# Kernel optimization log

Hardware: AMD Instinct MI355X
Metric: run time of the kernel (lower is better)

Reference implementation:

```python
import jax, jax.numpy as jnp
import numpy as np

N = 100000      # nodes
E = 1600000     # edges
C_IN = 128
H = 64          # hidden_channels
FC = [128, 64, 32, 16]
G = 64          # graphs in batch
EPS = 1e-5


def _glorot(key, fan_in, fan_out):
    s = 1.0 / np.sqrt(fan_in)
    return jax.random.uniform(key, (fan_in, fan_out), jnp.float32, -s, s)


def setup_inputs() -> dict:
    key = jax.random.key(0)
    ks = jax.random.split(key, 24)
    inp = {
        "x": jax.random.normal(ks[0], (N, C_IN), jnp.float32),
        "edge_index": jax.random.randint(ks[1], (2, E), 0, N, jnp.int32),
        "batch": jnp.sort(jax.random.randint(ks[2], (N,), 0, G, jnp.int32)),
        # GCN layers
        "W1": _glorot(ks[3], C_IN, H), "b1": jnp.zeros((H,), jnp.float32),
        "W2": _glorot(ks[4], H, H),    "b2": jnp.zeros((H,), jnp.float32),
        # BatchNorm affine params
        "gamma1": jnp.ones((H,), jnp.float32), "beta1": jnp.zeros((H,), jnp.float32),
        "gamma2": jnp.ones((H,), jnp.float32), "beta2": jnp.zeros((H,), jnp.float32),
        # MLP stack 64->128->64->32->16->1
        "fW1": _glorot(ks[5], H, FC[0]),     "fb1": jnp.zeros((FC[0],), jnp.float32),
        "fW2": _glorot(ks[6], FC[0], FC[1]), "fb2": jnp.zeros((FC[1],), jnp.float32),
        "fW3": _glorot(ks[7], FC[1], FC[2]), "fb3": jnp.zeros((FC[2],), jnp.float32),
        "fW4": _glorot(ks[8], FC[2], FC[3]), "fb4": jnp.zeros((FC[3],), jnp.float32),
        "oW": _glorot(ks[9], FC[3], 1),      "ob": jnp.zeros((1,), jnp.float32),
    }
    return inp


def gcn_conv(x, W, b, src, dst):
    # x' = D^{-1/2} (A + I) D^{-1/2} X W + b   (PyG GCNConv, add_self_loops=True)
    h = x @ W                                             # [N, H]
    loops = jnp.arange(N, dtype=src.dtype)
    s = jnp.concatenate([src, loops])
    d = jnp.concatenate([dst, loops])
    deg = jax.ops.segment_sum(jnp.ones_like(d, jnp.float32), d, num_segments=N)
    dinv = jax.lax.rsqrt(deg)                             # deg >= 1 (self-loops)
    norm = dinv[s] * dinv[d]                              # [E+N]
    msg = h[s] * norm[:, None]                            # gather + scale
    return jax.ops.segment_sum(msg, d, num_segments=N) + b


def batch_norm(x, gamma, beta):
    mu = jnp.mean(x, axis=0)
    var = jnp.mean((x - mu) ** 2, axis=0)                 # biased, as torch BN
    return (x - mu) * jax.lax.rsqrt(var + EPS) * gamma + beta


def reference(x, edge_index, batch, W1, b1, W2, b2, gamma1, beta1, gamma2, beta2,
              fW1, fb1, fW2, fb2, fW3, fb3, fW4, fb4, oW, ob):
    src, dst = edge_index[0], edge_index[1]
    h = jax.nn.relu(gcn_conv(x, W1, b1, src, dst))
    h = batch_norm(h, gamma1, beta1)                      # dropout = identity (eval)
    h = jax.nn.relu(gcn_conv(h, W2, b2, src, dst))
    h = batch_norm(h, gamma2, beta2)
    # global mean pool over graphs
    sums = jax.ops.segment_sum(h, batch, num_segments=G)
    cnts = jax.ops.segment_sum(jnp.ones((N,), jnp.float32), batch, num_segments=G)
    g = sums / jnp.maximum(cnts, 1.0)[:, None]            # [G, H]
    g = jax.nn.relu(g @ fW1 + fb1)
    g = jax.nn.relu(g @ fW2 + fb2)
    g = jax.nn.relu(g @ fW3 + fb3)
    g = jax.nn.relu(g @ fW4 + fb4)
    return g @ oW + ob                                    # [G, 1]
```

## Files before the change

### kernel.cpp

```cpp
#include <hip/hip_runtime.h>
#include <hip/hip_bf16.h>
#include <hip/hip_fp16.h>

#define NNODES 100000
#define NEDGES 1600000
#define NGRAPH 64
#define NCOPY  32
#define NSLOT  8

#define CAP     48
#define NGEMM1  1563

#define PSH     9
#define PSZ2    512
#define NP2     196
#define PCAP    9216
#define EPB     4096
#define NBP1    391

__global__ __launch_bounds__(1024) void k_bucket(const int* __restrict__ ei,
                                                 unsigned* __restrict__ pstage,
                                                 unsigned* __restrict__ pcur) {
    const int tid = threadIdx.x;
    __shared__ unsigned lcnt[NP2];
    __shared__ unsigned lbase[NP2];
    if (tid < NP2) lcnt[tid] = 0u;
    __syncthreads();

    int e = blockIdx.x * EPB + tid * 4;
    bool valid = (e < NEDGES);
    unsigned v0=0,v1=0,v2=0,v3=0, p0=0,p1=0,p2=0,p3=0, o0=0,o1=0,o2=0,o3=0;
    if (valid) {
        int4 sv = *reinterpret_cast<const int4*>(&ei[e]);
        int4 dv = *reinterpret_cast<const int4*>(&ei[NEDGES + e]);
        unsigned d;
        d = (unsigned)dv.x; p0 = d >> PSH; v0 = ((d & (PSZ2-1u)) << 17) | (unsigned)sv.x; o0 = atomicAdd(&lcnt[p0], 1u);
        d = (unsigned)dv.y; p1 = d >> PSH; v1 = ((d & (PSZ2-1u)) << 17) | (unsigned)sv.y; o1 = atomicAdd(&lcnt[p1], 1u);
        d = (unsigned)dv.z; p2 = d >> PSH; v2 = ((d & (PSZ2-1u)) << 17) | (unsigned)sv.z; o2 = atomicAdd(&lcnt[p2], 1u);
        d = (unsigned)dv.w; p3 = d >> PSH; v3 = ((d & (PSZ2-1u)) << 17) | (unsigned)sv.w; o3 = atomicAdd(&lcnt[p3], 1u);
    }
    __syncthreads();
    if (tid < NP2) {
        unsigned c = lcnt[tid];
        lbase[tid] = c ? atomicAdd(&pcur[tid], c) : 0u;
    }
    __syncthreads();
    if (valid) {
        unsigned i0 = lbase[p0] + o0; if (i0 < PCAP) pstage[(size_t)p0 * PCAP + i0] = v0;
        unsigned i1 = lbase[p1] + o1; if (i1 < PCAP) pstage[(size_t)p1 * PCAP + i1] = v1;
        unsigned i2 = lbase[p2] + o2; if (i2 < PCAP) pstage[(size_t)p2 * PCAP + i2] = v2;
        unsigned i3 = lbase[p3] + o3; if (i3 < PCAP) pstage[(size_t)p3 * PCAP + i3] = v3;
    }
}

__global__ __launch_bounds__(1024) void k_build(const unsigned* __restrict__ pstage,
                                                const unsigned* __restrict__ pcur,
                                                unsigned* __restrict__ cnt,
                                                float* __restrict__ dinv,
                                                unsigned* __restrict__ colidx) {
    const int p   = blockIdx.x;
    const int tid = threadIdx.x;
    __shared__ unsigned cl[PSZ2];
    if (tid < PSZ2) cl[tid] = 0u;
    __syncthreads();
    unsigned nedge = min(pcur[p], (unsigned)PCAP);
    const unsigned* q = &pstage[(size_t)p * PCAP];
    for (unsigned i = tid; i < nedge; i += 1024) {
        unsigned v    = q[i];
        unsigned r    = v >> 17;
        unsigned src  = v & 0x1FFFFu;
        unsigned slot = atomicAdd(&cl[r], 1u);
        unsigned node = ((unsigned)p << PSH) + r;
        if (slot < CAP) colidx[node * CAP + slot] = src;
    }
    __syncthreads();
    if (tid < PSZ2) {
        unsigned node = ((unsigned)p << PSH) + (unsigned)tid;
        if (node < NNODES) {
            unsigned c = cl[tid];
            cnt[node]  = c;
            dinv[node] = rsqrtf((float)(c + 1u));
        }
    }
}

__global__ __launch_bounds__(256) void k_gemm1(const float* __restrict__ A,
                                               const float* __restrict__ W,
                                               const float* __restrict__ rowscale,
                                               __half* __restrict__ hd) {
    __shared__ float wlds[64 * 64];
    __shared__ float alds[64 * 68];
    const int tid = threadIdx.x;
    const int tc = (tid & 15) * 4;
    const int tr = (tid >> 4) * 4;
    const int row0 = blockIdx.x * 64;
    float acc[4][4];
    #pragma unroll
    for (int i = 0; i < 4; ++i)
        #pragma unroll
        for (int j = 0; j < 4; ++j) acc[i][j] = 0.f;

    for (int kc = 0; kc < 2; ++kc) {
        for (int idx2 = tid; idx2 < 64 * 16; idx2 += 256) {
            int r = idx2 >> 4, kk = (idx2 & 15) * 4;
            *reinterpret_cast<float4*>(&wlds[r * 64 + kk]) =
                *reinterpret_cast<const float4*>(&W[(kc * 64 + r) * 64 + kk]);
        }
        for (int idx2 = tid; idx2 < 64 * 16; idx2 += 256) {
            int r = idx2 >> 4, kk = (idx2 & 15) * 4;
            int row = row0 + r;
            float4 v = make_float4(0.f, 0.f, 0.f, 0.f);
            if (row < NNODES) v = *reinterpret_cast<const float4*>(&A[row * 128 + kc * 64 + kk]);
            *reinterpret_cast<float4*>(&alds[r * 68 + kk]) = v;
        }
        __syncthreads();
        #pragma unroll 8
        for (int k = 0; k < 64; ++k) {
            float4 wv = *reinterpret_cast<const float4*>(&wlds[k * 64 + tc]);
            float av[4];
            #pragma unroll
            for (int i = 0; i < 4; ++i) av[i] = alds[(tr + i) * 68 + k];
            #pragma unroll
            for (int i = 0; i < 4; ++i) {
                acc[i][0] = fmaf(av[i], wv.x, acc[i][0]);
                acc[i][1] = fmaf(av[i], wv.y, acc[i][1]);
                acc[i][2] = fmaf(av[i], wv.z, acc[i][2]);
                acc[i][3] = fmaf(av[i], wv.w, acc[i][3]);
            }
        }
        __syncthreads();
    }
    #pragma unroll
    for (int i = 0; i < 4; ++i) {
        int row = row0 + tr + i;
        if (row < NNODES) {
            float f = rowscale[row];
            __half2* p = reinterpret_cast<__half2*>(&hd[(size_t)row * 64 + tc]);
            p[0] = __floats2half2_rn(acc[i][0] * f, acc[i][1] * f);
            p[1] = __floats2half2_rn(acc[i][2] * f, acc[i][3] * f);
        }
    }
}

__device__ __forceinline__ void acc_row(const __half* __restrict__ hd, unsigned s, int c0, float4& acc) {
    uint2 u = *reinterpret_cast<const uint2*>(&hd[(size_t)s * 64 + c0]);
    __half2 x01 = *reinterpret_cast<__half2*>(&u.x);
    __half2 x23 = *reinterpret_cast<__half2*>(&u.y);
    float2 f01 = __half22float2(x01);
    float2 f23 = __half22float2(x23);
    acc.x += f01.x; acc.y += f01.y; acc.z += f23.x; acc.w += f23.y;
}

#define WAVE_REDUCE_8(s0,s1,s2,s3,q0,q1,q2,q3)                      \
    {                                                                \
        _Pragma("unroll")                                            \
        for (int m = 16; m < 64; m <<= 1) {                          \
            s0 += __shfl_xor(s0, m); s1 += __shfl_xor(s1, m);        \
            s2 += __shfl_xor(s2, m); s3 += __shfl_xor(s3, m);        \
            q0 += __shfl_xor(q0, m); q1 += __shfl_xor(q1, m);        \
            q2 += __shfl_xor(q2, m); q3 += __shfl_xor(q3, m);        \
        }                                                            \
    }

__global__ __launch_bounds__(256) void k_gather_fused(const unsigned* __restrict__ cnt,
                                                      const unsigned* __restrict__ colidx,
                                                      const __half* __restrict__ hd,
                                                      const float* __restrict__ dinv,
                                                      const float* __restrict__ bias,
                                                      float* __restrict__ act,
                                                      float* bn_sum, float* bn_sq, int n) {
    const int tid = threadIdx.x;
    const int grp = tid >> 4;
    const int c0  = (tid & 15) * 4;
    float4 bv = *reinterpret_cast<const float4*>(&bias[c0]);
    float s0=0.f,s1=0.f,s2=0.f,s3=0.f, q0=0.f,q1=0.f,q2=0.f,q3=0.f;

    #pragma unroll
    for (int it = 0; it < 2; ++it) {
        int node = blockIdx.x * 32 + grp * 2 + it;
        if (node < n) {
            unsigned deg = cnt[node];
            unsigned lo = (unsigned)node * CAP;
            unsigned hi = lo + deg;
            float4 acc = make_float4(0.f, 0.f, 0.f, 0.f);
            acc_row(hd, (unsigned)node, c0, acc);
            unsigned j = lo;
            for (; j + 4 <= hi; j += 4) {
                uint4 a = *reinterpret_cast<const uint4*>(&colidx[j]);
                acc_row(hd, a.x, c0, acc);
                acc_row(hd, a.y, c0, acc);
                acc_row(hd, a.z, c0, acc);
                acc_row(hd, a.w, c0, acc);
            }
            for (; j < hi; ++j) acc_row(hd, colidx[j], c0, acc);
            float w = dinv[node];
            float4 r;
            r.x = fmaxf(fmaf(acc.x, w, bv.x), 0.f);
            r.y = fmaxf(fmaf(acc.y, w, bv.y), 0.f);
            r.z = fmaxf(fmaf(acc.z, w, bv.z), 0.f);
            r.w = fmaxf(fmaf(acc.w, w, bv.w), 0.f);
            *reinterpret_cast<float4*>(&act[(size_t)node * 64 + c0]) = r;
            s0 += r.x; s1 += r.y; s2 += r.z; s3 += r.w;
            q0 = fmaf(r.x, r.x, q0); q1 = fmaf(r.y, r.y, q1);
            q2 = fmaf(r.z, r.z, q2); q3 = fmaf(r.w, r.w, q3);
        }
    }

    WAVE_REDUCE_8(s0,s1,s2,s3,q0,q1,q2,q3);
    __shared__ float ls[4 * 64];
    __shared__ float lq[4 * 64];
    int lane = tid & 63, wid = tid >> 6;
    if (lane < 16) {
        *reinterpret_cast<float4*>(&ls[wid * 64 + lane * 4]) = make_float4(s0, s1, s2, s3);
        *reinterpret_cast<float4*>(&lq[wid * 64 + lane * 4]) = make_float4(q0, q1, q2, q3);
    }
    __syncthreads();
    if (tid < 64) {
        int cpy = (blockIdx.x & (NCOPY - 1)) * 64;
        float S = ls[tid] + ls[64 + tid] + ls[128 + tid] + ls[192 + tid];
        float Q = lq[tid] + lq[64 + tid] + lq[128 + tid] + lq[192 + tid];
        atomicAdd(&bn_sum[cpy + tid], S);
        atomicAdd(&bn_sq[cpy + tid],  Q);
    }
}

__global__ __launch_bounds__(256) void k_gather_pool(const unsigned* __restrict__ cnt,
                                                     const unsigned* __restrict__ colidx,
                                                     const __half* __restrict__ hd,
                                                     const float* __restrict__ dinv,
                                                     const float* __restrict__ bias,
                                                     const int* __restrict__ batch,
                                                     float* __restrict__ gsum,
                                                     float* bn_sum, float* bn_sq, int n) {
    const int tid = threadIdx.x;
    const int grp = tid >> 4;
    const int c0  = (tid & 15) * 4;
    float4 bv = *reinterpret_cast<const float4*>(&bias[c0]);
    float s0=0.f,s1=0.f,s2=0.f,s3=0.f, q0=0.f,q1=0.f,q2=0.f,q3=0.f;

    __shared__ float lds_pool[NSLOT * 64];
    for (int i = tid; i < NSLOT * 64; i += 256) lds_pool[i] = 0.f;
    int node0 = blockIdx.x * 32;
    int g0 = batch[node0 < n ? node0 : (n - 1)];
    __syncthreads();

    #pragma unroll
    for (int it = 0; it < 2; ++it) {
        int node = node0 + grp * 2 + it;
        if (node < n) {
            unsigned deg = cnt[node];
            unsigned lo = (unsigned)node * CAP;
            unsigned hi = lo + deg;
            float4 acc = make_float4(0.f, 0.f, 0.f, 0.f);
            acc_row(hd, (unsigned)node, c0, acc);
            unsigned j = lo;
            for (; j + 4 <= hi; j += 4) {
                uint4 a = *reinterpret_cast<const uint4*>(&colidx[j]);
                acc_row(hd, a.x, c0, acc);
                acc_row(hd, a.y, c0, acc);
                acc_row(hd, a.z, c0, acc);
                acc_row(hd, a.w, c0, acc);
            }
            for (; j < hi; ++j) acc_row(hd, colidx[j], c0, acc);
            float w = dinv[node];
            float4 r;
            r.x = fmaxf(fmaf(acc.x, w, bv.x), 0.f);
            r.y = fmaxf(fmaf(acc.y, w, bv.y), 0.f);
            r.z = fmaxf(fmaf(acc.z, w, bv.z), 0.f);
            r.w = fmaxf(fmaf(acc.w, w, bv.w), 0.f);
            s0 += r.x; s1 += r.y; s2 += r.z; s3 += r.w;
            q0 = fmaf(r.x, r.x, q0); q1 = fmaf(r.y, r.y, q1);
            q2 = fmaf(r.z, r.z, q2); q3 = fmaf(r.w, r.w, q3);
            int slot = batch[node] - g0;
            if (slot < NSLOT) {
                atomicAdd(&lds_pool[slot * 64 + c0 + 0], r.x);
                atomicAdd(&lds_pool[slot * 64 + c0 + 1], r.y);
                atomicAdd(&lds_pool[slot * 64 + c0 + 2], r.z);
                atomicAdd(&lds_pool[slot * 64 + c0 + 3], r.w);
            } else {
                int g = g0 + slot;
                atomicAdd(&gsum[g * 64 + c0 + 0], r.x);
                atomicAdd(&gsum[g * 64 + c0 + 1], r.y);
                atomicAdd(&gsum[g * 64 + c0 + 2], r.z);
                atomicAdd(&gsum[g * 64 + c0 + 3], r.w);
            }
        }
    }

    WAVE_REDUCE_8(s0,s1,s2,s3,q0,q1,q2,q3);
    __shared__ float ls[4 * 64];
    __shared__ float lq[4 * 64];
    int lane = tid & 63, wid = tid >> 6;
    if (lane < 16) {
        *reinterpret_cast<float4*>(&ls[wid * 64 + lane * 4]) = make_float4(s0, s1, s2, s3);
        *reinterpret_cast<float4*>(&lq[wid * 64 + lane * 4]) = make_float4(q0, q1, q2, q3);
    }
    __syncthreads();
    if (tid < 64) {
        int cpy = (blockIdx.x & (NCOPY - 1)) * 64;
        float S = ls[tid] + ls[64 + tid] + ls[128 + tid] + ls[192 + tid];
        float Q = lq[tid] + lq[64 + tid] + lq[128 + tid] + lq[192 + tid];
        atomicAdd(&bn_sum[cpy + tid], S);
        atomicAdd(&bn_sq[cpy + tid],  Q);
        #pragma unroll
        for (int sl = 0; sl < NSLOT; ++sl) {
            int g = g0 + sl;
            if (g < NGRAPH) {
                float v = lds_pool[sl * 64 + tid];
                if (v != 0.f) atomicAdd(&gsum[g * 64 + tid], v);
            }
        }
    }
}

__global__ void k_bn_fold_w2(const float* __restrict__ bn_sum, const float* __restrict__ bn_sq,
                             const float* __restrict__ gamma, const float* __restrict__ beta,
                             const float* __restrict__ W2, float* __restrict__ W2eff,
                             float* __restrict__ c2, int n) {
    __shared__ float sc[64], sh[64];
    int t = threadIdx.x;
    float S = 0.f, Q = 0.f;
    #pragma unroll
    for (int cpy = 0; cpy < NCOPY; ++cpy) { S += bn_sum[cpy * 64 + t]; Q += bn_sq[cpy * 64 + t]; }
    float inv_n = 1.0f / (float)n;
    float mu  = S * inv_n;
    float var = Q * inv_n - mu * mu;
    float s = gamma[t] * rsqrtf(var + 1e-5f);
    sc[t] = s; sh[t] = beta[t] - mu * s;
    __syncthreads();
    float acc = 0.f;
    for (int k = 0; k < 64; ++k) {
        float w = W2[k * 64 + t];
        W2eff[k * 64 + t] = sc[k] * w;
        acc = fmaf(sh[k], w, acc);
    }
    c2[t] = acc;
}

__global__ __launch_bounds__(256) void k_gemm64_h(const float* __restrict__ A,
                                                  const float* __restrict__ W,
                                                  const float* __restrict__ addvec,
                                                  const float* __restrict__ rowscale,
                                                  __half* __restrict__ hd, int n) {
    __shared__ float wlds[64 * 64];
    __shared__ float alds[64 * 68];
    const int tid = threadIdx.x;
    const int tc  = (tid & 15) * 4;
    const int tr  = (tid >> 4) * 4;
    const int row0 = blockIdx.x * 64;

    float acc[4][4];
    float4 cv = *reinterpret_cast<const float4*>(&addvec[tc]);
    #pragma unroll
    for (int i = 0; i < 4; ++i) { acc[i][0]=cv.x; acc[i][1]=cv.y; acc[i][2]=cv.z; acc[i][3]=cv.w; }

    {
        for (int idx = tid; idx < 64 * 16; idx += 256) {
            int r = idx >> 4, kk = (idx & 15) * 4;
            *reinterpret_cast<float4*>(&wlds[r * 64 + kk]) =
                *reinterpret_cast<const float4*>(&W[r * 64 + kk]);
        }
        for (int idx = tid; idx < 64 * 16; idx += 256) {
            int r = idx >> 4, kk = (idx & 15) * 4;
            int row = row0 + r;
            float4 v = make_float4(0.f, 0.f, 0.f, 0.f);
            if (row < n) v = *reinterpret_cast<const float4*>(&A[row * 64 + kk]);
            *reinterpret_cast<float4*>(&alds[r * 68 + kk]) = v;
        }
        __syncthreads();
        #pragma unroll 8
        for (int k = 0; k < 64; ++k) {
            float4 wv = *reinterpret_cast<const float4*>(&wlds[k * 64 + tc]);
            float av[4];
            #pragma unroll
            for (int i = 0; i < 4; ++i) av[i] = alds[(tr + i) * 68 + k];
            #pragma unroll
            for (int i = 0; i < 4; ++i) {
                acc[i][0] = fmaf(av[i], wv.x, acc[i][0]);
                acc[i][1] = fmaf(av[i], wv.y, acc[i][1]);
                acc[i][2] = fmaf(av[i], wv.z, acc[i][2]);
                acc[i][3] = fmaf(av[i], wv.w, acc[i][3]);
            }
        }
    }
    #pragma unroll
    for (int i = 0; i < 4; ++i) {
        int row = row0 + tr + i;
        if (row < n) {
            float f = rowscale[row];
            __half2* p = reinterpret_cast<__half2*>(&hd[(size_t)row * 64 + tc]);
            p[0] = __floats2half2_rn(acc[i][0] * f, acc[i][1] * f);
            p[1] = __floats2half2_rn(acc[i][2] * f, acc[i][3] * f);
        }
    }
}

__device__ __forceinline__ int lower_bound_i(const int* a, int n, int v) {
    int lo = 0, hi = n;
    while (lo < hi) { int m = (lo + hi) >> 1; if (a[m] < v) lo = m + 1; else hi = m; }
    return lo;
}
__global__ __launch_bounds__(128) void k_mlp(const float* __restrict__ gsum,
                                             const int* __restrict__ batch, int n,
                                             const float* __restrict__ bn_sum, const float* __restrict__ bn_sq,
                                             const float* __restrict__ gamma, const float* __restrict__ beta,
                                             const float* __restrict__ fW1, const float* __restrict__ fb1,
                                             const float* __restrict__ fW2, const float* __restrict__ fb2,
                                             const float* __restrict__ fW3, const float* __restrict__ fb3,
                                             const float* __restrict__ fW4, const float* __restrict__ fb4,
                                             const float* __restrict__ oW,  const float* __restrict__ ob,
                                             float* __restrict__ out) {
    int g = blockIdx.x;
    int t = threadIdx.x;
    __shared__ float a[128], bbuf[128];
    if (t < 64) {
        float S = 0.f, Q = 0.f;
        #pragma unroll
        for (int cpy = 0; cpy < NCOPY; ++cpy) { S += bn_sum[cpy * 64 + t]; Q += bn_sq[cpy * 64 + t]; }
        float inv_n = 1.0f / (float)n;
        float mu  = S * inv_n;
        float var = Q * inv_n - mu * mu;
        float s   = gamma[t] * rsqrtf(var + 1e-5f);
        float sh  = beta[t] - mu * s;
        int lo = lower_bound_i(batch, n, g);
        int hi = lower_bound_i(batch, n, g + 1);
        int cnt = hi - lo;
        a[t] = (cnt > 0) ? (gsum[g * 64 + t] / (float)cnt) * s + sh : 0.f;
    }
    __syncthreads();
    {
        float acc = fb1[t];
        for (int k = 0; k < 64; ++k) acc = fmaf(a[k], fW1[k * 128 + t], acc);
        bbuf[t] = fmaxf(acc, 0.f);
    }
    __syncthreads();
    if (t < 64) {
        float acc = fb2[t];
        for (int k = 0; k < 128; ++k) acc = fmaf(bbuf[k], fW2[k * 64 + t], acc);
        a[t] = fmaxf(acc, 0.f);
    }
    __syncthreads();
    if (t < 32) {
        float acc = fb3[t];
        for (int k = 0; k < 64; ++k) acc = fmaf(a[k], fW3[k * 32 + t], acc);
        bbuf[t] = fmaxf(acc, 0.f);
    }
    __syncthreads();
    if (t < 16) {
        float acc = fb4[t];
        for (int k = 0; k < 32; ++k) acc = fmaf(bbuf[k], fW4[k * 16 + t], acc);
        a[t] = fmaxf(acc, 0.f);
    }
    __syncthreads();
    if (t == 0) {
        float acc = ob[0];
        for (int k = 0; k < 16; ++k) acc = fmaf(a[k], oW[k], acc);
        out[g] = acc;
    }
}

extern "C" void kernel_launch(void* const* d_in, const int* in_sizes, int n_in,
                              void* d_out, int out_size, void* d_ws, size_t ws_size,
                              hipStream_t stream) {
    const float* x      = (const float*)d_in[0];
    const int*   ei     = (const int*)  d_in[1];
    const int*   batch  = (const int*)  d_in[2];
    const float* W1     = (const float*)d_in[3];
    const float* b1     = (const float*)d_in[4];
    const float* W2     = (const float*)d_in[5];
    const float* b2     = (const float*)d_in[6];
    const float* gamma1 = (const float*)d_in[7];
    const float* beta1  = (const float*)d_in[8];
    const float* gamma2 = (const float*)d_in[9];
    const float* beta2  = (const float*)d_in[10];
    const float* fW1    = (const float*)d_in[11];
    const float* fb1    = (const float*)d_in[12];
    const float* fW2    = (const float*)d_in[13];
    const float* fb2    = (const float*)d_in[14];
    const float* fW3    = (const float*)d_in[15];
    const float* fb3    = (const float*)d_in[16];
    const float* fW4    = (const float*)d_in[17];
    const float* fb4    = (const float*)d_in[18];
    const float* oW     = (const float*)d_in[19];
    const float* ob     = (const float*)d_in[20];
    float* out = (float*)d_out;

    const int N = NNODES, G = NGRAPH;

    char* base = (char*)d_ws;
    __half*   hd     = (__half*)base;
    float*    act    = (float*)(base + (size_t)N * 64 * 2);
    unsigned* cnt    = (unsigned*)((char*)act + (size_t)N * 64 * 4);
    float*    dinv   = (float*)(cnt + N);
    unsigned* colidx = (unsigned*)(dinv + N);
    float*    bn1s   = (float*)(colidx + (size_t)N * CAP);
    float*    bn1q   = bn1s + NCOPY * 64;
    float*    bn2s   = bn1q + NCOPY * 64;
    float*    bn2q   = bn2s + NCOPY * 64;
    float*    gsum   = bn2q + NCOPY * 64;
    float*    W2eff  = gsum + (size_t)G * 64;
    float*    c2     = W2eff + 4096;
    unsigned* pcur   = (unsigned*)(c2 + 64);
    unsigned* pstage = (unsigned*)act;

    hipMemsetAsync(pcur, 0, (size_t)NP2 * 4, stream);
    hipMemsetAsync(bn1s, 0, (size_t)(4 * NCOPY * 64 + G * 64) * sizeof(float), stream);

    k_bucket<<<NBP1, 1024, 0, stream>>>(ei, pstage, pcur);
    k_build<<<NP2, 1024, 0, stream>>>(pstage, pcur, cnt, dinv, colidx);

    k_gemm1<<<NGEMM1, 256, 0, stream>>>(x, W1, dinv, hd);

    k_gather_fused<<<(N + 31) / 32, 256, 0, stream>>>(cnt, colidx, hd, dinv, b1, act, bn1s, bn1q, N);
    k_bn_fold_w2<<<1, 64, 0, stream>>>(bn1s, bn1q, gamma1, beta1, W2, W2eff, c2, N);

    k_gemm64_h<<<(N + 63) / 64, 256, 0, stream>>>(act, W2eff, c2, dinv, hd, N);
    k_gather_pool<<<(N + 31) / 32, 256, 0, stream>>>(cnt, colidx, hd, dinv, b2, batch, gsum, bn2s, bn2q, N);

    k_mlp<<<G, 128, 0, stream>>>(gsum, batch, N, bn2s, bn2q, gamma2, beta2,
                                 fW1, fb1, fW2, fb2, fW3, fb3, fW4, fb4, oW, ob, out);
}
```

Baseline: 309.2 us.

## Fuse edge bucketing with GEMM1, fold BN into GEMM2, store activations in fp16

Edge bucketing and the first GEMM now run in one launch, with odd blocks doing the bucketing and even blocks doing the GEMM. Because GEMM1 no longer waits for the degree array, its source-side dinv scaling moves into the gather, which does one extra dinv load per edge. The BatchNorm fold kernel is merged into the second GEMM, and each block recomputes the scaled weights. The intermediate activation is stored in fp16 instead of fp32 to halve its traffic, and the memsets are merged. This cuts launches and serialization but adds per-edge work in the gather and some extra rounding.

```diff
diff --git a/kernel.cpp b/kernel.cpp
--- a/kernel.cpp
+++ b/kernel.cpp
@@ -15,85 +15,55 @@
 #define PSZ2    512
 #define NP2     196
 #define PCAP    9216
-#define EPB     4096
-#define NBP1    391
-
-__global__ __launch_bounds__(1024) void k_bucket(const int* __restrict__ ei,
-                                                 unsigned* __restrict__ pstage,
-                                                 unsigned* __restrict__ pcur) {
+
+__global__ __launch_bounds__(256) void k_bucket_gemm1(const float* __restrict__ A,
+                                                      const float* __restrict__ W,
+                                                      const int* __restrict__ ei,
+                                                      unsigned* __restrict__ pstage,
+                                                      unsigned* __restrict__ pcur,
+                                                      __half* __restrict__ hd) {
+    __shared__ __align__(16) float smem[64 * 64 + 64 * 68];
+    const int b   = blockIdx.x;
     const int tid = threadIdx.x;
-    __shared__ unsigned lcnt[NP2];
-    __shared__ unsigned lbase[NP2];
-    if (tid < NP2) lcnt[tid] = 0u;
-    __syncthreads();
-
-    int e = blockIdx.x * EPB + tid * 4;
-    bool valid = (e < NEDGES);
-    unsigned v0=0,v1=0,v2=0,v3=0, p0=0,p1=0,p2=0,p3=0, o0=0,o1=0,o2=0,o3=0;
-    if (valid) {
-        int4 sv = *reinterpret_cast<const int4*>(&ei[e]);
-        int4 dv = *reinterpret_cast<const int4*>(&ei[NEDGES + e]);
-        unsigned d;
-        d = (unsigned)dv.x; p0 = d >> PSH; v0 = ((d & (PSZ2-1u)) << 17) | (unsigned)sv.x; o0 = atomicAdd(&lcnt[p0], 1u);
-        d = (unsigned)dv.y; p1 = d >> PSH; v1 = ((d & (PSZ2-1u)) << 17) | (unsigned)sv.y; o1 = atomicAdd(&lcnt[p1], 1u);
-        d = (unsigned)dv.z; p2 = d >> PSH; v2 = ((d & (PSZ2-1u)) << 17) | (unsigned)sv.z; o2 = atomicAdd(&lcnt[p2], 1u);
-        d = (unsigned)dv.w; p3 = d >> PSH; v3 = ((d & (PSZ2-1u)) << 17) | (unsigned)sv.w; o3 = atomicAdd(&lcnt[p3], 1u);
-    }
-    __syncthreads();
-    if (tid < NP2) {
-        unsigned c = lcnt[tid];
-        lbase[tid] = c ? atomicAdd(&pcur[tid], c) : 0u;
-    }
-    __syncthreads();
-    if (valid) {
-        unsigned i0 = lbase[p0] + o0; if (i0 < PCAP) pstage[(size_t)p0 * PCAP + i0] = v0;
-        unsigned i1 = lbase[p1] + o1; if (i1 < PCAP) pstage[(size_t)p1 * PCAP + i1] = v1;
-        unsigned i2 = lbase[p2] + o2; if (i2 < PCAP) pstage[(size_t)p2 * PCAP + i2] = v2;
-        unsigned i3 = lbase[p3] + o3; if (i3 < PCAP) pstage[(size_t)p3 * PCAP + i3] = v3;
-    }
-}
-
-__global__ __launch_bounds__(1024) void k_build(const unsigned* __restrict__ pstage,
-                                                const unsigned* __restrict__ pcur,
-                                                unsigned* __restrict__ cnt,
-                                                float* __restrict__ dinv,
-                                                unsigned* __restrict__ colidx) {
-    const int p   = blockIdx.x;
-    const int tid = threadIdx.x;
-    __shared__ unsigned cl[PSZ2];
-    if (tid < PSZ2) cl[tid] = 0u;
-    __syncthreads();
-    unsigned nedge = min(pcur[p], (unsigned)PCAP);
-    const unsigned* q = &pstage[(size_t)p * PCAP];
-    for (unsigned i = tid; i < nedge; i += 1024) {
-        unsigned v    = q[i];
-        unsigned r    = v >> 17;
-        unsigned src  = v & 0x1FFFFu;
-        unsigned slot = atomicAdd(&cl[r], 1u);
-        unsigned node = ((unsigned)p << PSH) + r;
-        if (slot < CAP) colidx[node * CAP + slot] = src;
-    }
-    __syncthreads();
-    if (tid < PSZ2) {
-        unsigned node = ((unsigned)p << PSH) + (unsigned)tid;
-        if (node < NNODES) {
-            unsigned c = cl[tid];
-            cnt[node]  = c;
-            dinv[node] = rsqrtf((float)(c + 1u));
-        }
-    }
-}
-
-__global__ __launch_bounds__(256) void k_gemm1(const float* __restrict__ A,
-                                               const float* __restrict__ W,
-                                               const float* __restrict__ rowscale,
-                                               __half* __restrict__ hd) {
-    __shared__ float wlds[64 * 64];
-    __shared__ float alds[64 * 68];
-    const int tid = threadIdx.x;
+
+    if (b & 1) {
+        unsigned* lcnt  = reinterpret_cast<unsigned*>(smem);
+        unsigned* lbase = lcnt + 256;
+        if (tid < NP2) lcnt[tid] = 0u;
+        __syncthreads();
+
+        int e = (b >> 1) * 1024 + tid * 4;
+        bool valid = (e < NEDGES);
+        unsigned v0=0,v1=0,v2=0,v3=0, p0=0,p1=0,p2=0,p3=0, o0=0,o1=0,o2=0,o3=0;
+        if (valid) {
+            int4 sv = *reinterpret_cast<const int4*>(&ei[e]);
+            int4 dv = *reinterpret_cast<const int4*>(&ei[NEDGES + e]);
+            unsigned d;
+            d = (unsigned)dv.x; p0 = d >> PSH; v0 = ((d & (PSZ2-1u)) << 17) | (unsigned)sv.x; o0 = atomicAdd(&lcnt[p0], 1u);
+            d = (unsigned)dv.y; p1 = d >> PSH; v1 = ((d & (PSZ2-1u)) << 17) | (unsigned)sv.y; o1 = atomicAdd(&lcnt[p1], 1u);
+            d = (unsigned)dv.z; p2 = d >> PSH; v2 = ((d & (PSZ2-1u)) << 17) | (unsigned)sv.z; o2 = atomicAdd(&lcnt[p2], 1u);
+            d = (unsigned)dv.w; p3 = d >> PSH; v3 = ((d & (PSZ2-1u)) << 17) | (unsigned)sv.w; o3 = atomicAdd(&lcnt[p3], 1u);
+        }
+        __syncthreads();
+        if (tid < NP2) {
+            unsigned c = lcnt[tid];
+            lbase[tid] = c ? atomicAdd(&pcur[tid], c) : 0u;
+        }
+        __syncthreads();
+        if (valid) {
+            unsigned i0 = lbase[p0] + o0; if (i0 < PCAP) pstage[(size_t)p0 * PCAP + i0] = v0;
+            unsigned i1 = lbase[p1] + o1; if (i1 < PCAP) pstage[(size_t)p1 * PCAP + i1] = v1;
+            unsigned i2 = lbase[p2] + o2; if (i2 < PCAP) pstage[(size_t)p2 * PCAP + i2] = v2;
+            unsigned i3 = lbase[p3] + o3; if (i3 < PCAP) pstage[(size_t)p3 * PCAP + i3] = v3;
+        }
+        return;
+    }
+
+    float* wlds = smem;
+    float* alds = smem + 64 * 64;
     const int tc = (tid & 15) * 4;
     const int tr = (tid >> 4) * 4;
-    const int row0 = blockIdx.x * 64;
+    const int row0 = (b >> 1) * 64;
     float acc[4][4];
     #pragma unroll
     for (int i = 0; i < 4; ++i)
@@ -110,7 +80,7 @@
             int r = idx2 >> 4, kk = (idx2 & 15) * 4;
             int row = row0 + r;
             float4 v = make_float4(0.f, 0.f, 0.f, 0.f);
-            if (row < NNODES) v = *reinterpret_cast<const float4*>(&A[row * 128 + kc * 64 + kk]);
+            if (row < NNODES) v = *reinterpret_cast<const float4*>(&A[(size_t)row * 128 + kc * 64 + kk]);
             *reinterpret_cast<float4*>(&alds[r * 68 + kk]) = v;
         }
         __syncthreads();
@@ -134,10 +104,40 @@
     for (int i = 0; i < 4; ++i) {
         int row = row0 + tr + i;
         if (row < NNODES) {
-            float f = rowscale[row];
             __half2* p = reinterpret_cast<__half2*>(&hd[(size_t)row * 64 + tc]);
-            p[0] = __floats2half2_rn(acc[i][0] * f, acc[i][1] * f);
-            p[1] = __floats2half2_rn(acc[i][2] * f, acc[i][3] * f);
+            p[0] = __floats2half2_rn(acc[i][0], acc[i][1]);
+            p[1] = __floats2half2_rn(acc[i][2], acc[i][3]);
+        }
+    }
+}
+
+__global__ __launch_bounds__(1024) void k_build(const unsigned* __restrict__ pstage,
+                                                const unsigned* __restrict__ pcur,
+                                                unsigned* __restrict__ cnt,
+                                                float* __restrict__ dinv,
+                                                unsigned* __restrict__ colidx) {
+    const int p   = blockIdx.x;
+    const int tid = threadIdx.x;
+    __shared__ unsigned cl[PSZ2];
+    if (tid < PSZ2) cl[tid] = 0u;
+    __syncthreads();
+    unsigned nedge = min(pcur[p], (unsigned)PCAP);
+    const unsigned* q = &pstage[(size_t)p * PCAP];
+    for (unsigned i = tid; i < nedge; i += 1024) {
+        unsigned v    = q[i];
+        unsigned r    = v >> 17;
+        unsigned src  = v & 0x1FFFFu;
+        unsigned slot = atomicAdd(&cl[r], 1u);
+        unsigned node = ((unsigned)p << PSH) + r;
+        if (slot < CAP) colidx[node * CAP + slot] = src;
+    }
+    __syncthreads();
+    if (tid < PSZ2) {
+        unsigned node = ((unsigned)p << PSH) + (unsigned)tid;
+        if (node < NNODES) {
+            unsigned c = cl[tid];
+            cnt[node]  = c;
+            dinv[node] = rsqrtf((float)(c + 1u));
         }
     }
 }
@@ -149,6 +149,17 @@
     float2 f01 = __half22float2(x01);
     float2 f23 = __half22float2(x23);
     acc.x += f01.x; acc.y += f01.y; acc.z += f23.x; acc.w += f23.y;
+}
+__device__ __forceinline__ void acc_row_s(const __half* __restrict__ hd, const float* __restrict__ dinv,
+                                          unsigned s, int c0, float4& acc) {
+    float ds = dinv[s];
+    uint2 u = *reinterpret_cast<const uint2*>(&hd[(size_t)s * 64 + c0]);
+    __half2 x01 = *reinterpret_cast<__half2*>(&u.x);
+    __half2 x23 = *reinterpret_cast<__half2*>(&u.y);
+    float2 f01 = __half22float2(x01);
+    float2 f23 = __half22float2(x23);
+    acc.x = fmaf(f01.x, ds, acc.x); acc.y = fmaf(f01.y, ds, acc.y);
+    acc.z = fmaf(f23.x, ds, acc.z); acc.w = fmaf(f23.y, ds, acc.w);
 }
 
 #define WAVE_REDUCE_8(s0,s1,s2,s3,q0,q1,q2,q3)                      \
@@ -167,7 +178,7 @@
                                                       const __half* __restrict__ hd,
                                                       const float* __restrict__ dinv,
                                                       const float* __restrict__ bias,
-                                                      float* __restrict__ act,
+                                                      __half* __restrict__ acth,
                                                       float* bn_sum, float* bn_sq, int n) {
     const int tid = threadIdx.x;
     const int grp = tid >> 4;
@@ -183,23 +194,25 @@
             unsigned lo = (unsigned)node * CAP;
             unsigned hi = lo + deg;
             float4 acc = make_float4(0.f, 0.f, 0.f, 0.f);
-            acc_row(hd, (unsigned)node, c0, acc);
+            acc_row_s(hd, dinv, (unsigned)node, c0, acc);
             unsigned j = lo;
             for (; j + 4 <= hi; j += 4) {
                 uint4 a = *reinterpret_cast<const uint4*>(&colidx[j]);
-                acc_row(hd, a.x, c0, acc);
-                acc_row(hd, a.y, c0, acc);
-                acc_row(hd, a.z, c0, acc);
-                acc_row(hd, a.w, c0, acc);
+                acc_row_s(hd, dinv, a.x, c0, acc);
+                acc_row_s(hd, dinv, a.y, c0, acc);
+                acc_row_s(hd, dinv, a.z, c0, acc);
+                acc_row_s(hd, dinv, a.w, c0, acc);
             }
-            for (; j < hi; ++j) acc_row(hd, colidx[j], c0, acc);
+            for (; j < hi; ++j) acc_row_s(hd, dinv, colidx[j], c0, acc);
             float w = dinv[node];
             float4 r;
             r.x = fmaxf(fmaf(acc.x, w, bv.x), 0.f);
             r.y = fmaxf(fmaf(acc.y, w, bv.y), 0.f);
             r.z = fmaxf(fmaf(acc.z, w, bv.z), 0.f);
             r.w = fmaxf(fmaf(acc.w, w, bv.w), 0.f);
-            *reinterpret_cast<float4*>(&act[(size_t)node * 64 + c0]) = r;
+            __half2* pa = reinterpret_cast<__half2*>(&acth[(size_t)node * 64 + c0]);
+            pa[0] = __floats2half2_rn(r.x, r.y);
+            pa[1] = __floats2half2_rn(r.z, r.w);
             s0 += r.x; s1 += r.y; s2 += r.z; s3 += r.w;
             q0 = fmaf(r.x, r.x, q0); q1 = fmaf(r.y, r.y, q1);
             q2 = fmaf(r.z, r.z, q2); q3 = fmaf(r.w, r.w, q3);
@@ -221,6 +234,89 @@
         float Q = lq[tid] + lq[64 + tid] + lq[128 + tid] + lq[192 + tid];
         atomicAdd(&bn_sum[cpy + tid], S);
         atomicAdd(&bn_sq[cpy + tid],  Q);
+    }
+}
+
+__global__ __launch_bounds__(256) void k_gemm2_fold(const __half* __restrict__ A,
+                                                    const float* __restrict__ W2,
+                                                    const float* __restrict__ bn_sum,
+                                                    const float* __restrict__ bn_sq,
+                                                    const float* __restrict__ gamma,
+                                                    const float* __restrict__ beta,
+                                                    const float* __restrict__ rowscale,
+                                                    __half* __restrict__ hd, int n) {
+    __shared__ float wlds[64 * 64];
+    __shared__ float alds[64 * 68];
+    __shared__ float scs[64], shs[64], c2s[64];
+    const int tid = threadIdx.x;
+    const int tc  = (tid & 15) * 4;
+    const int tr  = (tid >> 4) * 4;
+    const int row0 = blockIdx.x * 64;
+
+    if (tid < 64) {
+        float S = 0.f, Q = 0.f;
+        #pragma unroll
+        for (int cpy = 0; cpy < NCOPY; ++cpy) { S += bn_sum[cpy * 64 + tid]; Q += bn_sq[cpy * 64 + tid]; }
+        float inv_n = 1.0f / (float)n;
+        float mu  = S * inv_n;
+        float var = Q * inv_n - mu * mu;
+        float s = gamma[tid] * rsqrtf(var + 1e-5f);
+        scs[tid] = s; shs[tid] = beta[tid] - mu * s;
+    }
+    __syncthreads();
+    for (int idx = tid; idx < 4096; idx += 256) {
+        int k = idx >> 6;
+        wlds[idx] = scs[k] * W2[idx];
+    }
+    if (tid < 64) {
+        float acc = 0.f;
+        for (int k = 0; k < 64; ++k) acc = fmaf(shs[k], W2[k * 64 + tid], acc);
+        c2s[tid] = acc;
+    }
+    for (int idx = tid; idx < 64 * 16; idx += 256) {
+        int r = idx >> 4, kk = (idx & 15) * 4;
+        int row = row0 + r;
+        float4 v = make_float4(0.f, 0.f, 0.f, 0.f);
+        if (row < n) {
+            uint2 u = *reinterpret_cast<const uint2*>(&A[(size_t)row * 64 + kk]);
+            __half2 h01 = *reinterpret_cast<__half2*>(&u.x);
+            __half2 h23 = *reinterpret_cast<__half2*>(&u.y);
+            float2 f01 = __half22float2(h01);
+            float2 f23 = __half22float2(h23);
+            v = make_float4(f01.x, f01.y, f23.x, f23.y);
+        }
+        *reinterpret_cast<float4*>(&alds[r * 68 + kk]) = v;
+    }
+    __syncthreads();
+
+    float acc[4][4];
+    float4 cv = make_float4(c2s[tc], c2s[tc + 1], c2s[tc + 2], c2s[tc + 3]);
+    #pragma unroll
+    for (int i = 0; i < 4; ++i) { acc[i][0]=cv.x; acc[i][1]=cv.y; acc[i][2]=cv.z; acc[i][3]=cv.w; }
+
+    #pragma unroll 8
+    for (int k = 0; k < 64; ++k) {
+        float4 wv = *reinterpret_cast<const float4*>(&wlds[k * 64 + tc]);
+        float av[4];
+        #pragma unroll
+        for (int i = 0; i < 4; ++i) av[i] = alds[(tr + i) * 68 + k];
+        #pragma unroll
+        for (int i = 0; i < 4; ++i) {
+            acc[i][0] = fmaf(av[i], wv.x, acc[i][0]);
+            acc[i][1] = fmaf(av[i], wv.y, acc[i][1]);
+            acc[i][2] = fmaf(av[i], wv.z, acc[i][2]);
+            acc[i][3] = fmaf(av[i], wv.w, acc[i][3]);
+        }
+    }
+    #pragma unroll
+    for (int i = 0; i < 4; ++i) {
+        int row = row0 + tr + i;
+        if (row < n) {
+            float f = rowscale[row];
+            __half2* p = reinterpret_cast<__half2*>(&hd[(size_t)row * 64 + tc]);
+            p[0] = __floats2half2_rn(acc[i][0] * f, acc[i][1] * f);
+            p[1] = __floats2half2_rn(acc[i][2] * f, acc[i][3] * f);
+        }
     }
 }
 
@@ -313,88 +409,6 @@
     }
 }
 
-__global__ void k_bn_fold_w2(const float* __restrict__ bn_sum, const float* __restrict__ bn_sq,
-                             const float* __restrict__ gamma, const float* __restrict__ beta,
-                             const float* __restrict__ W2, float* __restrict__ W2eff,
-                             float* __restrict__ c2, int n) {
-    __shared__ float sc[64], sh[64];
-    int t = threadIdx.x;
-    float S = 0.f, Q = 0.f;
-    #pragma unroll
-    for (int cpy = 0; cpy < NCOPY; ++cpy) { S += bn_sum[cpy * 64 + t]; Q += bn_sq[cpy * 64 + t]; }
-    float inv_n = 1.0f / (float)n;
-    float mu  = S * inv_n;
-    float var = Q * inv_n - mu * mu;
-    float s = gamma[t] * rsqrtf(var + 1e-5f);
-    sc[t] = s; sh[t] = beta[t] - mu * s;
-    __syncthreads();
-    float acc = 0.f;
-    for (int k = 0; k < 64; ++k) {
-        float w = W2[k * 64 + t];
-        W2eff[k * 64 + t] = sc[k] * w;
-        acc = fmaf(sh[k], w, acc);
-    }
-    c2[t] = acc;
-}
-
-__global__ __launch_bounds__(256) void k_gemm64_h(const float* __restrict__ A,
-                                                  const float* __restrict__ W,
-                                                  const float* __restrict__ addvec,
-                                                  const float* __restrict__ rowscale,
-                                                  __half* __restrict__ hd, int n) {
-    __shared__ float wlds[64 * 64];
-    __shared__ float alds[64 * 68];
-    const int tid = threadIdx.x;
-    const int tc  = (tid & 15) * 4;
-    const int tr  = (tid >> 4) * 4;
-    const int row0 = blockIdx.x * 64;
-
-    float acc[4][4];
-    float4 cv = *reinterpret_cast<const float4*>(&addvec[tc]);
-    #pragma unroll
-    for (int i = 0; i < 4; ++i) { acc[i][0]=cv.x; acc[i][1]=cv.y; acc[i][2]=cv.z; acc[i][3]=cv.w; }
-
-    {
-        for (int idx = tid; idx < 64 * 16; idx += 256) {
-            int r = idx >> 4, kk = (idx & 15) * 4;
-            *reinterpret_cast<float4*>(&wlds[r * 64 + kk]) =
-                *reinterpret_cast<const float4*>(&W[r * 64 + kk]);
-        }
-        for (int idx = tid; idx < 64 * 16; idx += 256) {
-            int r = idx >> 4, kk = (idx & 15) * 4;
-            int row = row0 + r;
-            float4 v = make_float4(0.f, 0.f, 0.f, 0.f);
-            if (row < n) v = *reinterpret_cast<const float4*>(&A[row * 64 + kk]);
-            *reinterpret_cast<float4*>(&alds[r * 68 + kk]) = v;
-        }
-        __syncthreads();
-        #pragma unroll 8
-        for (int k = 0; k < 64; ++k) {
-            float4 wv = *reinterpret_cast<const float4*>(&wlds[k * 64 + tc]);
-            float av[4];
-            #pragma unroll
-            for (int i = 0; i < 4; ++i) av[i] = alds[(tr + i) * 68 + k];
-            #pragma unroll
-            for (int i = 0; i < 4; ++i) {
-                acc[i][0] = fmaf(av[i], wv.x, acc[i][0]);
-                acc[i][1] = fmaf(av[i], wv.y, acc[i][1]);
-                acc[i][2] = fmaf(av[i], wv.z, acc[i][2]);
-                acc[i][3] = fmaf(av[i], wv.w, acc[i][3]);
-            }
-        }
-    }
-    #pragma unroll
-    for (int i = 0; i < 4; ++i) {
-        int row = row0 + tr + i;
-        if (row < n) {
-            float f = rowscale[row];
-            __half2* p = reinterpret_cast<__half2*>(&hd[(size_t)row * 64 + tc]);
-            p[0] = __floats2half2_rn(acc[i][0] * f, acc[i][1] * f);
-            p[1] = __floats2half2_rn(acc[i][2] * f, acc[i][3] * f);
-        }
-    }
-}
-
 __device__ __forceinline__ int lower_bound_i(const int* a, int n, int v) {
     int lo = 0, hi = n;
     while (lo < hi) { int m = (lo + hi) >> 1; if (a[m] < v) lo = m + 1; else hi = m; }
@@ -489,8 +503,8 @@
 
     char* base = (char*)d_ws;
     __half*   hd     = (__half*)base;
-    float*    act    = (float*)(base + (size_t)N * 64 * 2);
-    unsigned* cnt    = (unsigned*)((char*)act + (size_t)N * 64 * 4);
+    __half*   acth   = (__half*)(base + (size_t)N * 64 * 2);
+    unsigned* cnt    = (unsigned*)(base + (size_t)N * 64 * 4);
     float*    dinv   = (float*)(cnt + N);
     unsigned* colidx = (unsigned*)(dinv + N);
     float*    bn1s   = (float*)(colidx + (size_t)N * CAP);
@@ -498,23 +512,20 @@
     float*    bn2s   = bn1q + NCOPY * 64;
     float*    bn2q   = bn2s + NCOPY * 64;
     float*    gsum   = bn2q + NCOPY * 64;
-    float*    W2eff  = gsum + (size_t)G * 64;
-    float*    c2     = W2eff + 4096;
-    unsigned* pcur   = (unsigned*)(c2 + 64);
-    unsigned* pstage = (unsigned*)act;
-
-    hipMemsetAsync(pcur, 0, (size_t)NP2 * 4, stream);
-    hipMemsetAsync(bn1s, 0, (size_t)(4 * NCOPY * 64 + G * 64) * sizeof(float), stream);
-
-    k_bucket<<<NBP1, 1024, 0, stream>>>(ei, pstage, pcur);
+    unsigned* pcur   = (unsigned*)(gsum + (size_t)G * 64);
+    const size_t ZBYTES = (size_t)(4 * NCOPY * 64 + G * 64) * 4 + (size_t)NP2 * 4;
+    unsigned* pstage = (unsigned*)acth;
+
+    hipMemsetAsync(bn1s, 0, ZBYTES, stream);
+
+    k_bucket_gemm1<<<2 * NGEMM1, 256, 0, stream>>>(x, W1, ei, pstage, pcur, hd);
+
     k_build<<<NP2, 1024, 0, stream>>>(pstage, pcur, cnt, dinv, colidx);
 
-    k_gemm1<<<NGEMM1, 256, 0, stream>>>(x, W1, dinv, hd);
-
-    k_gather_fused<<<(N + 31) / 32, 256, 0, stream>>>(cnt, colidx, hd, dinv, b1, act, bn1s, bn1q, N);
-    k_bn_fold_w2<<<1, 64, 0, stream>>>(bn1s, bn1q, gamma1, beta1, W2, W2eff, c2, N);
-
-    k_gemm64_h<<<(N + 63) / 64, 256, 0, stream>>>(act, W2eff, c2, dinv, hd, N);
+    k_gather_fused<<<(N + 31) / 32, 256, 0, stream>>>(cnt, colidx, hd, dinv, b1, acth, bn1s, bn1q, N);
+
+    k_gemm2_fold<<<NGEMM1, 256, 0, stream>>>(acth, W2, bn1s, bn1q, gamma1, beta1, dinv, hd, N);
+
     k_gather_pool<<<(N + 31) / 32, 256, 0, stream>>>(cnt, colidx, hd, dinv, b2, batch, gsum, bn2s, bn2q, N);
 
     k_mlp<<<G, 128, 0, stream>>>(gsum, batch, N, bn2s, bn2q, gamma2, beta2,
```

Result: no change. 306.1 us (-1.0%).
